# Performance work log

Measured on AMD Instinct MI355X. Metric: run time of the kernel, lower is better.

Reference implementation:

```python
import jax, jax.numpy as jnp
import numpy as np

D_MODEL = 512
NUM_HEADS = 8
DEPTH = D_MODEL // NUM_HEADS
PROJ_DIM = 256
SEQ_LEN = 4096
BATCH = 8


def _glorot(key, shape):
    fan_in, fan_out = shape[-2], shape[-1]
    limit = np.sqrt(6.0 / (fan_in + fan_out))
    return jax.random.uniform(key, shape, jnp.float32, -limit, limit)


def setup_inputs() -> dict:
    key = jax.random.key(0)
    ks = jax.random.split(key, 8)
    x = jax.random.normal(ks[0], (BATCH, SEQ_LEN, D_MODEL), jnp.float32)
    wq = _glorot(ks[1], (D_MODEL, D_MODEL))
    wk = _glorot(ks[2], (D_MODEL, D_MODEL))
    wv = _glorot(ks[3], (D_MODEL, D_MODEL))
    E = _glorot(ks[4], (NUM_HEADS, SEQ_LEN, PROJ_DIM))
    F = _glorot(ks[5], (NUM_HEADS, SEQ_LEN, PROJ_DIM))
    w_out = _glorot(ks[6], (D_MODEL, D_MODEL))
    b_out = jnp.zeros((D_MODEL,), jnp.float32)
    return {"x": x, "wq": wq, "wk": wk, "wv": wv, "E": E, "F": F,
            "w_out": w_out, "b_out": b_out}


def reference(x, wq, wk, wv, E, F, w_out, b_out):
    b, n, _ = x.shape
    # QKV projections + split heads -> [b, h, n, d]
    def split_heads(t):
        return t.reshape(b, n, NUM_HEADS, DEPTH).transpose(0, 2, 1, 3)
    q = split_heads(x @ wq)
    k = split_heads(x @ wk)
    v = split_heads(x @ wv)
    # Linformer low-rank projection of K/V along sequence: [b,h,r,d]
    k_proj = jnp.einsum('bhnd,hnr->bhrd', k, E)
    v_proj = jnp.einsum('bhnd,hnr->bhrd', v, F)
    scale = 1.0 / jnp.sqrt(jnp.asarray(DEPTH, jnp.float32))
    scores = jnp.einsum('bhnd,bhrd->bhnr', q, k_proj) * scale  # [b,h,n,r]
    attn = jax.nn.softmax(scores, axis=-1)
    out = jnp.einsum('bhnr,bhrd->bhnd', attn, v_proj)
    out = out.transpose(0, 2, 1, 3).reshape(b, n, D_MODEL)
    return out @ w_out + b_out
```

## Files before the change

kernel.cpp:

```cpp
#include <hip/hip_runtime.h>

typedef unsigned short u16;
typedef unsigned int   u32;
typedef __bf16 bf16x8 __attribute__((ext_vector_type(8)));
typedef float  f32x4  __attribute__((ext_vector_type(4)));
typedef u16    u16x4  __attribute__((ext_vector_type(4)));

#define DEV __device__ __forceinline__

DEV u16 f2bf(float f) {
    u32 u = __builtin_bit_cast(u32, f);
    u = (u + 0x7fffu + ((u >> 16) & 1u)) >> 16;
    return (u16)u;
}

DEV void gload16(const void* g, void* l) {
    __builtin_amdgcn_global_load_lds((const __attribute__((address_space(1))) u32*)g,
                                     (__attribute__((address_space(3))) u32*)l, 16, 0, 0);
}


__global__ __launch_bounds__(256) void k_cvt4(const float* __restrict__ in,
                                              u16* __restrict__ out, int n) {
    int i = ((int)blockIdx.x * 256 + (int)threadIdx.x) * 4;
    if (i < n) {
        float4 v = *(const float4*)(in + i);
        u16x4 o;
        o[0] = f2bf(v.x); o[1] = f2bf(v.y); o[2] = f2bf(v.z); o[3] = f2bf(v.w);
        *(u16x4*)(out + i) = o;
    }
}

__global__ __launch_bounds__(256) void k_wt(const float* __restrict__ wq, const float* __restrict__ wk,
                                            const float* __restrict__ wv, const float* __restrict__ wo,
                                            u16* __restrict__ wcatT, u16* __restrict__ woT) {
    int idx = (int)blockIdx.x * 256 + (int)threadIdx.x;
    if (idx < 786432) {
        int j = idx >> 9, k = idx & 511;
        const float* w = (j < 512) ? wq : ((j < 1024) ? wk : wv);
        wcatT[idx] = f2bf(w[k * 512 + (j & 511)]);
    } else {
        int t = idx - 786432;
        int j = t >> 9, k = t & 511;
        woT[t] = f2bf(wo[k * 512 + j]);
    }
}

__global__ __launch_bounds__(256) void k_tef(const float* __restrict__ E, const float* __restrict__ F,
                                             u16* __restrict__ Et, u16* __restrict__ Ft) {
    __shared__ u16 tile[64][65];
    const int t = threadIdx.x;
    const int bid = blockIdx.x;
    const int rt = bid & 3, ntl = (bid >> 2) & 63, h = (bid >> 8) & 7, which = bid >> 11;
    const float* src = (which ? F : E) + (size_t)h * 4096 * 256;
    u16* dst = (which ? Ft : Et) + (size_t)h * 256 * 4096;
    const int n0 = ntl * 64, r0 = rt * 64;
#pragma unroll
    for (int it = 0; it < 16; ++it) {
        const int idx = t + it * 256;
        const int nl = idx >> 6, rl = idx & 63;
        tile[nl][rl] = f2bf(src[(size_t)(n0 + nl) * 256 + r0 + rl]);
    }
    __syncthreads();
#pragma unroll
    for (int it = 0; it < 16; ++it) {
        const int idx = t + it * 256;
        const int rl = idx >> 6, nl = idx & 63;
        dst[(size_t)(r0 + rl) * 4096 + n0 + nl] = tile[nl][rl];
    }
}

template <int MODE>
__global__ __launch_bounds__(256) void k_gemm(const u16* __restrict__ A, const u16* __restrict__ Bm,
                                              u16* __restrict__ Qo, u16* __restrict__ Kt, u16* __restrict__ Vt,
                                              float* __restrict__ Of, const float* __restrict__ bias,
                                              int M, int N, int K) {
    __shared__ __attribute__((aligned(16))) char smem[32768];
    const int tid = threadIdx.x;
    const int lane = tid & 63, wid = tid >> 6;
    const int wr = wid >> 1, wc = wid & 1;
    const int g = lane >> 4, l16 = lane & 15;
    const int nM = M >> 7;
    const int bm = (int)blockIdx.x % nM, bn = (int)blockIdx.x / nM;
    const int m0 = bm << 7, n0 = bn << 7;

    f32x4 acc[4][4] = {};

    for (int k0 = 0; k0 < K; k0 += 64) {
#pragma unroll
        for (int c = 0; c < 4; ++c) {
            const int off = c * 4096 + tid * 16;
            const int row = off >> 7;
            const int sc = ((off >> 4) & 7) ^ (row & 7);
            gload16(A  + (size_t)(m0 + row) * K + (k0 + sc * 8), smem + off);
            gload16(Bm + (size_t)(n0 + row) * K + (k0 + sc * 8), smem + 16384 + off);
        }
        __syncthreads();
#pragma unroll
        for (int kk = 0; kk < 64; kk += 32) {
            bf16x8 av[4], bv[4];
#pragma unroll
            for (int m = 0; m < 4; ++m) {
                const int r = wr * 64 + m * 16 + l16;
                av[m] = *(const bf16x8*)(smem + r * 128 + ((kk * 2 + g * 16) ^ ((r & 7) << 4)));
            }
#pragma unroll
            for (int n = 0; n < 4; ++n) {
                const int r = wc * 64 + n * 16 + l16;
                bv[n] = *(const bf16x8*)(smem + 16384 + r * 128 + ((kk * 2 + g * 16) ^ ((r & 7) << 4)));
            }
#pragma unroll
            for (int m = 0; m < 4; ++m)
#pragma unroll
                for (int n = 0; n < 4; ++n)
                    acc[m][n] = __builtin_amdgcn_mfma_f32_16x16x32_bf16(av[m], bv[n], acc[m][n], 0, 0, 0);
        }
        __syncthreads();
    }

    if (MODE == 0) {
        if (n0 < 512) {
#pragma unroll
            for (int m = 0; m < 4; ++m)
#pragma unroll
                for (int n = 0; n < 4; ++n) {
                    const int col = n0 + wc * 64 + n * 16 + l16;
#pragma unroll
                    for (int i = 0; i < 4; ++i) {
                        const int row = m0 + wr * 64 + m * 16 + g * 4 + i;
                        Qo[(size_t)row * 512 + col] = f2bf(acc[m][n][i]);
                    }
                }
        } else {
            u16* dst = (n0 < 1024) ? Kt : Vt;
#pragma unroll
            for (int m = 0; m < 4; ++m)
#pragma unroll
                for (int n = 0; n < 4; ++n) {
                    const int col = (n0 + wc * 64 + n * 16 + l16) & 511;
                    const int h = col >> 6, d = col & 63;
                    const int rowb = m0 + wr * 64 + m * 16 + g * 4;
                    const int b = rowb >> 12, nn = rowb & 4095;
                    u16x4 pk;
#pragma unroll
                    for (int i = 0; i < 4; ++i) pk[i] = f2bf(acc[m][n][i]);
                    *(u16x4*)(dst + ((size_t)((b * 8 + h) * 64 + d)) * 4096 + nn) = pk;
                }
        }
    } else {
#pragma unroll
        for (int m = 0; m < 4; ++m)
#pragma unroll
            for (int n = 0; n < 4; ++n) {
                const int col = n0 + wc * 64 + n * 16 + l16;
                const float bb = bias[col];
#pragma unroll
                for (int i = 0; i < 4; ++i) {
                    const int row = m0 + wr * 64 + m * 16 + g * 4 + i;
                    Of[(size_t)row * N + col] = acc[m][n][i] + bb;
                }
            }
    }
}

__global__ __launch_bounds__(256) void k_proj(const u16* __restrict__ Et, const u16* __restrict__ Ft,
                                              const u16* __restrict__ Kt, const u16* __restrict__ Vt,
                                              u16* __restrict__ kp, u16* __restrict__ vpT) {
    __shared__ __attribute__((aligned(16))) char smem[24576];
    const int tid = threadIdx.x;
    const int lane = tid & 63, wid = tid >> 6;
    const int wr = wid >> 1, wc = wid & 1;
    const int g = lane >> 4, l16 = lane & 15;
    const int bid = blockIdx.x;
    const int mt = bid & 1, which = (bid >> 1) & 1, bh = bid >> 2;
    const int h = bh & 7;
    const u16* Ap = (which ? Ft : Et) + (size_t)h * 256 * 4096 + (size_t)mt * 128 * 4096;
    const u16* Bp = (which ? Vt : Kt) + (size_t)bh * 64 * 4096;

    f32x4 acc[4][2] = {};

    for (int k0 = 0; k0 < 4096; k0 += 64) {
#pragma unroll
        for (int c = 0; c < 4; ++c) {
            const int off = c * 4096 + tid * 16;
            const int row = off >> 7;
            const int sc = ((off >> 4) & 7) ^ (row & 7);
            gload16(Ap + (size_t)row * 4096 + (k0 + sc * 8), smem + off);
            if (c < 2)
                gload16(Bp + (size_t)row * 4096 + (k0 + sc * 8), smem + 16384 + off);
        }
        __syncthreads();
#pragma unroll
        for (int kk = 0; kk < 64; kk += 32) {
            bf16x8 av[4], bv[2];
#pragma unroll
            for (int m = 0; m < 4; ++m) {
                const int r = wr * 64 + m * 16 + l16;
                av[m] = *(const bf16x8*)(smem + r * 128 + ((kk * 2 + g * 16) ^ ((r & 7) << 4)));
            }
#pragma unroll
            for (int n = 0; n < 2; ++n) {
                const int r = wc * 32 + n * 16 + l16;
                bv[n] = *(const bf16x8*)(smem + 16384 + r * 128 + ((kk * 2 + g * 16) ^ ((r & 7) << 4)));
            }
#pragma unroll
            for (int m = 0; m < 4; ++m)
#pragma unroll
                for (int n = 0; n < 2; ++n)
                    acc[m][n] = __builtin_amdgcn_mfma_f32_16x16x32_bf16(av[m], bv[n], acc[m][n], 0, 0, 0);
        }
        __syncthreads();
    }

    if (which == 0) {
#pragma unroll
        for (int m = 0; m < 4; ++m)
#pragma unroll
            for (int n = 0; n < 2; ++n) {
                const int d = wc * 32 + n * 16 + l16;
#pragma unroll
                for (int i = 0; i < 4; ++i) {
                    const int rg = mt * 128 + wr * 64 + m * 16 + g * 4 + i;
                    kp[(size_t)bh * 16384 + rg * 64 + d] = f2bf(acc[m][n][i]);
                }
            }
    } else {
#pragma unroll
        for (int m = 0; m < 4; ++m)
#pragma unroll
            for (int n = 0; n < 2; ++n) {
                const int d = wc * 32 + n * 16 + l16;
                const int r4 = mt * 128 + wr * 64 + m * 16 + g * 4;
                u16x4 pk;
#pragma unroll
                for (int i = 0; i < 4; ++i) pk[i] = f2bf(acc[m][n][i]);
                *(u16x4*)(vpT + (size_t)bh * 16384 + d * 256 + r4) = pk;
            }
    }
}

__global__ __launch_bounds__(256) void k_flash(const u16* __restrict__ Q, const u16* __restrict__ kp,
                                               const u16* __restrict__ vpT, u16* __restrict__ ctx) {
    __shared__ __attribute__((aligned(16))) char smem[65536];
    const int tid = threadIdx.x;
    const int lane = tid & 63, w = tid >> 6;
    const int g = lane >> 4, l16 = lane & 15;
    const int bid = blockIdx.x;
    const int nt = bid & 63, bh = bid >> 6;
    const int b = bh >> 3, h = bh & 7;
    const int n0 = nt * 64;

#pragma unroll
    for (int c = 0; c < 8; ++c) {
        const int off = c * 4096 + tid * 16;
        {
            const int row = off >> 7;
            const int sc = ((off >> 4) & 7) ^ (row & 7);
            gload16(kp + (size_t)bh * 16384 + row * 64 + sc * 8, smem + off);
        }
        {
            const int row = off >> 9;
            const int sc = ((off >> 4) & 31) ^ (row & 7);
            gload16(vpT + (size_t)bh * 16384 + row * 256 + sc * 8, smem + 32768 + off);
        }
    }
    const size_t qbase = (size_t)(b * 4096 + n0 + w * 16 + l16) * 512 + h * 64 + g * 8;
    bf16x8 qf0 = *(const bf16x8*)(Q + qbase);
    bf16x8 qf1 = *(const bf16x8*)(Q + qbase + 32);
    __syncthreads();

    f32x4 s[16];
#pragma unroll
    for (int rt = 0; rt < 16; ++rt) {
        const int r = rt * 16 + l16;
        const int sw = (r & 7) << 4;
        bf16x8 kv0 = *(const bf16x8*)(smem + r * 128 + ((g * 16) ^ sw));
        bf16x8 kv1 = *(const bf16x8*)(smem + r * 128 + ((64 + g * 16) ^ sw));
        f32x4 z = {0.f, 0.f, 0.f, 0.f};
        z = __builtin_amdgcn_mfma_f32_16x16x32_bf16(qf0, kv0, z, 0, 0, 0);
        z = __builtin_amdgcn_mfma_f32_16x16x32_bf16(qf1, kv1, z, 0, 0, 0);
        s[rt] = z;
    }

    float mx[4] = {-1e30f, -1e30f, -1e30f, -1e30f};
#pragma unroll
    for (int rt = 0; rt < 16; ++rt)
#pragma unroll
        for (int i = 0; i < 4; ++i) {
            s[rt][i] *= 0.125f;
            mx[i] = fmaxf(mx[i], s[rt][i]);
        }
#pragma unroll
    for (int i = 0; i < 4; ++i) {
        mx[i] = fmaxf(mx[i], __shfl_xor(mx[i], 1));
        mx[i] = fmaxf(mx[i], __shfl_xor(mx[i], 2));
        mx[i] = fmaxf(mx[i], __shfl_xor(mx[i], 4));
        mx[i] = fmaxf(mx[i], __shfl_xor(mx[i], 8));
    }
    float sm[4] = {0.f, 0.f, 0.f, 0.f};
#pragma unroll
    for (int rt = 0; rt < 16; ++rt)
#pragma unroll
        for (int i = 0; i < 4; ++i) {
            float e = __expf(s[rt][i] - mx[i]);
            s[rt][i] = e;
            sm[i] += e;
        }
#pragma unroll
    for (int i = 0; i < 4; ++i) {
        sm[i] += __shfl_xor(sm[i], 1);
        sm[i] += __shfl_xor(sm[i], 2);
        sm[i] += __shfl_xor(sm[i], 4);
        sm[i] += __shfl_xor(sm[i], 8);
    }

    __syncthreads();

#pragma unroll
    for (int rt = 0; rt < 16; ++rt)
#pragma unroll
        for (int i = 0; i < 4; ++i) {
            const int nrow = g * 4 + i;
            const int byte = w * 8192 + nrow * 512 + ((rt * 32 + l16 * 2) ^ ((nrow & 7) << 4));
            *(u16*)(smem + byte) = f2bf(s[rt][i]);
        }
    bf16x8 af[8];
#pragma unroll
    for (int ks = 0; ks < 8; ++ks) {
        const int byte = w * 8192 + l16 * 512 + ((ks * 64 + g * 16) ^ ((l16 & 7) << 4));
        af[ks] = *(const bf16x8*)(smem + byte);
    }
    f32x4 o[4] = {};
#pragma unroll
    for (int dt = 0; dt < 4; ++dt)
#pragma unroll
        for (int ks = 0; ks < 8; ++ks) {
            const int row = dt * 16 + l16;
            const int byte = 32768 + row * 512 + ((ks * 64 + g * 16) ^ ((row & 7) << 4));
            bf16x8 bv = *(const bf16x8*)(smem + byte);
            o[dt] = __builtin_amdgcn_mfma_f32_16x16x32_bf16(af[ks], bv, o[dt], 0, 0, 0);
        }
    float rinv[4];
#pragma unroll
    for (int i = 0; i < 4; ++i) rinv[i] = 1.0f / sm[i];
#pragma unroll
    for (int dt = 0; dt < 4; ++dt)
#pragma unroll
        for (int i = 0; i < 4; ++i) {
            const int row = b * 4096 + n0 + w * 16 + g * 4 + i;
            const int col = h * 64 + dt * 16 + l16;
            ctx[(size_t)row * 512 + col] = f2bf(o[dt][i] * rinv[i]);
        }
}


extern "C" void kernel_launch(void* const* d_in, const int* in_sizes, int n_in,
                              void* d_out, int out_size, void* d_ws, size_t ws_size,
                              hipStream_t stream) {
    const float* x  = (const float*)d_in[0];
    const float* wq = (const float*)d_in[1];
    const float* wk = (const float*)d_in[2];
    const float* wv = (const float*)d_in[3];
    const float* E  = (const float*)d_in[4];
    const float* F  = (const float*)d_in[5];
    const float* wo = (const float*)d_in[6];
    const float* bo = (const float*)d_in[7];
    float* out = (float*)d_out;
    u16* ws = (u16*)d_ws;

    u16* xb    = ws;
    u16* Qm    = ws + 16777216;
    u16* Kt    = ws + 33554432;
    u16* Vt    = ws + 50331648;
    u16* Et    = ws + 67108864;
    u16* Ft    = ws + 75497472;
    u16* wcatT = ws + 83886080;
    u16* woT   = ws + 84672512;
    u16* kpB   = ws + 84934656;
    u16* vpT   = ws + 85983232;
    u16* ctx   = xb;

    k_cvt4<<<16384, 256, 0, stream>>>(x, xb, 16777216);
    k_wt<<<4096, 256, 0, stream>>>(wq, wk, wv, wo, wcatT, woT);
    k_tef<<<4096, 256, 0, stream>>>(E, F, Et, Ft);
    k_gemm<0><<<3072, 256, 0, stream>>>(xb, wcatT, Qm, Kt, Vt, nullptr, nullptr, 32768, 1536, 512);
    k_proj<<<256, 256, 0, stream>>>(Et, Ft, Kt, Vt, kpB, vpT);
    k_flash<<<4096, 256, 0, stream>>>(Qm, kpB, vpT, ctx);
    k_gemm<1><<<1024, 256, 0, stream>>>(ctx, woT, nullptr, nullptr, nullptr, out, bo, 32768, 512, 512);
}
```

Baseline: 400.6 us.

## Split-K Linformer projection, fuse prep kernels, remap GEMM tiles, add setprio

Splits the sequence-length reduction in k_proj into four chunks written as fp32 partials, then reduced and converted to bf16 by a new kernel, so the projection uses four times as many blocks. The three input-conversion kernels merge into one launch, and the weight transpose now uses an LDS tile for coalesced access. GEMM block indices are remapped so each XCD covers contiguous M tiles, and MFMA loops are wrapped in s_setprio. This adds an extra fp32 buffer pass and a reduction launch.

Measured after the change: 385.3 us. 3.8% less time.

```diff
diff --git a/kernel.cpp b/kernel.cpp
--- a/kernel.cpp
+++ b/kernel.cpp
@@ -19,54 +19,59 @@
                                      (__attribute__((address_space(3))) u32*)l, 16, 0, 0);
 }
 
-
-__global__ __launch_bounds__(256) void k_cvt4(const float* __restrict__ in,
-                                              u16* __restrict__ out, int n) {
-    int i = ((int)blockIdx.x * 256 + (int)threadIdx.x) * 4;
-    if (i < n) {
-        float4 v = *(const float4*)(in + i);
-        u16x4 o;
-        o[0] = f2bf(v.x); o[1] = f2bf(v.y); o[2] = f2bf(v.z); o[3] = f2bf(v.w);
-        *(u16x4*)(out + i) = o;
-    }
-}
-
-__global__ __launch_bounds__(256) void k_wt(const float* __restrict__ wq, const float* __restrict__ wk,
-                                            const float* __restrict__ wv, const float* __restrict__ wo,
-                                            u16* __restrict__ wcatT, u16* __restrict__ woT) {
-    int idx = (int)blockIdx.x * 256 + (int)threadIdx.x;
-    if (idx < 786432) {
-        int j = idx >> 9, k = idx & 511;
-        const float* w = (j < 512) ? wq : ((j < 1024) ? wk : wv);
-        wcatT[idx] = f2bf(w[k * 512 + (j & 511)]);
-    } else {
-        int t = idx - 786432;
-        int j = t >> 9, k = t & 511;
-        woT[t] = f2bf(wo[k * 512 + j]);
-    }
-}
-
-__global__ __launch_bounds__(256) void k_tef(const float* __restrict__ E, const float* __restrict__ F,
-                                             u16* __restrict__ Et, u16* __restrict__ Ft) {
+__global__ __launch_bounds__(256) void k_prep(const float* __restrict__ x,
+                                              const float* __restrict__ wq, const float* __restrict__ wk,
+                                              const float* __restrict__ wv, const float* __restrict__ wo,
+                                              const float* __restrict__ E, const float* __restrict__ F,
+                                              u16* __restrict__ xb, u16* __restrict__ wcatT, u16* __restrict__ woT,
+                                              u16* __restrict__ Et, u16* __restrict__ Ft) {
     __shared__ u16 tile[64][65];
     const int t = threadIdx.x;
     const int bid = blockIdx.x;
-    const int rt = bid & 3, ntl = (bid >> 2) & 63, h = (bid >> 8) & 7, which = bid >> 11;
-    const float* src = (which ? F : E) + (size_t)h * 4096 * 256;
-    u16* dst = (which ? Ft : Et) + (size_t)h * 256 * 4096;
-    const int n0 = ntl * 64, r0 = rt * 64;
-#pragma unroll
-    for (int it = 0; it < 16; ++it) {
-        const int idx = t + it * 256;
-        const int nl = idx >> 6, rl = idx & 63;
-        tile[nl][rl] = f2bf(src[(size_t)(n0 + nl) * 256 + r0 + rl]);
-    }
-    __syncthreads();
-#pragma unroll
-    for (int it = 0; it < 16; ++it) {
-        const int idx = t + it * 256;
-        const int rl = idx >> 6, nl = idx & 63;
-        dst[(size_t)(r0 + rl) * 4096 + n0 + nl] = tile[nl][rl];
+    if (bid < 16384) {
+        int i = (bid * 256 + t) * 4;
+        float4 v = *(const float4*)(x + i);
+        u16x4 o;
+        o[0] = f2bf(v.x); o[1] = f2bf(v.y); o[2] = f2bf(v.z); o[3] = f2bf(v.w);
+        *(u16x4*)(xb + i) = o;
+    } else if (bid < 20480) {
+        const int b2 = bid - 16384;
+        const int rt = b2 & 3, ntl = (b2 >> 2) & 63, h = (b2 >> 8) & 7, which = b2 >> 11;
+        const float* src = (which ? F : E) + (size_t)h * 4096 * 256;
+        u16* dst = (which ? Ft : Et) + (size_t)h * 256 * 4096;
+        const int n0 = ntl * 64, r0 = rt * 64;
+#pragma unroll
+        for (int it = 0; it < 16; ++it) {
+            const int idx = t + it * 256;
+            const int nl = idx >> 6, rl = idx & 63;
+            tile[nl][rl] = f2bf(src[(size_t)(n0 + nl) * 256 + r0 + rl]);
+        }
+        __syncthreads();
+#pragma unroll
+        for (int it = 0; it < 16; ++it) {
+            const int idx = t + it * 256;
+            const int rl = idx >> 6, nl = idx & 63;
+            dst[(size_t)(r0 + rl) * 4096 + n0 + nl] = tile[nl][rl];
+        }
+    } else {
+        const int b2 = bid - 20480;
+        const int mi = b2 >> 6, tix = b2 & 63;
+        const int jt = tix & 7, kt = tix >> 3;
+        const float* w = (mi == 0) ? wq : (mi == 1) ? wk : (mi == 2) ? wv : wo;
+        u16* dst = (mi < 3) ? (wcatT + mi * 262144) : woT;
+#pragma unroll
+        for (int it = 0; it < 16; ++it) {
+            const int idx = t + it * 256;
+            const int kl = idx >> 6, jl = idx & 63;
+            tile[kl][jl] = f2bf(w[(kt * 64 + kl) * 512 + jt * 64 + jl]);
+        }
+        __syncthreads();
+#pragma unroll
+        for (int it = 0; it < 16; ++it) {
+            const int idx = t + it * 256;
+            const int jl = idx >> 6, kl = idx & 63;
+            dst[(size_t)(jt * 64 + jl) * 512 + kt * 64 + kl] = tile[kl][jl];
+        }
     }
 }
 
@@ -80,8 +85,9 @@
     const int lane = tid & 63, wid = tid >> 6;
     const int wr = wid >> 1, wc = wid & 1;
     const int g = lane >> 4, l16 = lane & 15;
-    const int nM = M >> 7;
-    const int bm = (int)blockIdx.x % nM, bn = (int)blockIdx.x / nM;
+    const int bid = (int)blockIdx.x;
+    const int xcd = bid & 7, loc = bid >> 3;
+    const int bm = xcd * 32 + (loc & 31), bn = loc >> 5;
     const int m0 = bm << 7, n0 = bn << 7;
 
     f32x4 acc[4][4] = {};
@@ -109,11 +115,13 @@
                 const int r = wc * 64 + n * 16 + l16;
                 bv[n] = *(const bf16x8*)(smem + 16384 + r * 128 + ((kk * 2 + g * 16) ^ ((r & 7) << 4)));
             }
+            __builtin_amdgcn_s_setprio(1);
 #pragma unroll
             for (int m = 0; m < 4; ++m)
 #pragma unroll
                 for (int n = 0; n < 4; ++n)
                     acc[m][n] = __builtin_amdgcn_mfma_f32_16x16x32_bf16(av[m], bv[n], acc[m][n], 0, 0, 0);
+            __builtin_amdgcn_s_setprio(0);
         }
         __syncthreads();
     }
@@ -165,21 +173,23 @@
 
 __global__ __launch_bounds__(256) void k_proj(const u16* __restrict__ Et, const u16* __restrict__ Ft,
                                               const u16* __restrict__ Kt, const u16* __restrict__ Vt,
-                                              u16* __restrict__ kp, u16* __restrict__ vpT) {
+                                              float* __restrict__ pbuf) {
     __shared__ __attribute__((aligned(16))) char smem[24576];
     const int tid = threadIdx.x;
     const int lane = tid & 63, wid = tid >> 6;
     const int wr = wid >> 1, wc = wid & 1;
     const int g = lane >> 4, l16 = lane & 15;
     const int bid = blockIdx.x;
-    const int mt = bid & 1, which = (bid >> 1) & 1, bh = bid >> 2;
+    const int sp = bid >> 8, rest = bid & 255;
+    const int mt = rest & 1, which = (rest >> 1) & 1, bh = rest >> 2;
     const int h = bh & 7;
     const u16* Ap = (which ? Ft : Et) + (size_t)h * 256 * 4096 + (size_t)mt * 128 * 4096;
     const u16* Bp = (which ? Vt : Kt) + (size_t)bh * 64 * 4096;
 
     f32x4 acc[4][2] = {};
 
-    for (int k0 = 0; k0 < 4096; k0 += 64) {
+    const int kbeg = sp * 1024;
+    for (int k0 = kbeg; k0 < kbeg + 1024; k0 += 64) {
 #pragma unroll
         for (int c = 0; c < 4; ++c) {
             const int off = c * 4096 + tid * 16;
@@ -203,15 +213,18 @@
                 const int r = wc * 32 + n * 16 + l16;
                 bv[n] = *(const bf16x8*)(smem + 16384 + r * 128 + ((kk * 2 + g * 16) ^ ((r & 7) << 4)));
             }
+            __builtin_amdgcn_s_setprio(1);
 #pragma unroll
             for (int m = 0; m < 4; ++m)
 #pragma unroll
                 for (int n = 0; n < 2; ++n)
                     acc[m][n] = __builtin_amdgcn_mfma_f32_16x16x32_bf16(av[m], bv[n], acc[m][n], 0, 0, 0);
-        }
-        __syncthreads();
-    }
-
+            __builtin_amdgcn_s_setprio(0);
+        }
+        __syncthreads();
+    }
+
+    float* pb = pbuf + ((size_t)(sp * 2 + which) * 64 + bh) * 16384;
     if (which == 0) {
 #pragma unroll
         for (int m = 0; m < 4; ++m)
@@ -221,7 +234,7 @@
 #pragma unroll
                 for (int i = 0; i < 4; ++i) {
                     const int rg = mt * 128 + wr * 64 + m * 16 + g * 4 + i;
-                    kp[(size_t)bh * 16384 + rg * 64 + d] = f2bf(acc[m][n][i]);
+                    pb[rg * 64 + d] = acc[m][n][i];
                 }
             }
     } else {
@@ -231,12 +244,21 @@
             for (int n = 0; n < 2; ++n) {
                 const int d = wc * 32 + n * 16 + l16;
                 const int r4 = mt * 128 + wr * 64 + m * 16 + g * 4;
-                u16x4 pk;
-#pragma unroll
-                for (int i = 0; i < 4; ++i) pk[i] = f2bf(acc[m][n][i]);
-                *(u16x4*)(vpT + (size_t)bh * 16384 + d * 256 + r4) = pk;
-            }
-    }
+                *(f32x4*)(pb + d * 256 + r4) = acc[m][n];
+            }
+    }
+}
+
+__global__ __launch_bounds__(256) void k_preduce(const float* __restrict__ pbuf, u16* __restrict__ outkv) {
+    const int o = ((int)blockIdx.x * 256 + (int)threadIdx.x) * 4;
+    f32x4 s = *(const f32x4*)(pbuf + o);
+    s += *(const f32x4*)(pbuf + 2097152 + o);
+    s += *(const f32x4*)(pbuf + 4194304 + o);
+    s += *(const f32x4*)(pbuf + 6291456 + o);
+    u16x4 r;
+#pragma unroll
+    for (int i = 0; i < 4; ++i) r[i] = f2bf(s[i]);
+    *(u16x4*)(outkv + o) = r;
 }
 
 __global__ __launch_bounds__(256) void k_flash(const u16* __restrict__ Q, const u16* __restrict__ kp,
@@ -270,6 +292,7 @@
     __syncthreads();
 
     f32x4 s[16];
+    __builtin_amdgcn_s_setprio(1);
 #pragma unroll
     for (int rt = 0; rt < 16; ++rt) {
         const int r = rt * 16 + l16;
@@ -281,6 +304,7 @@
         z = __builtin_amdgcn_mfma_f32_16x16x32_bf16(qf1, kv1, z, 0, 0, 0);
         s[rt] = z;
     }
+    __builtin_amdgcn_s_setprio(0);
 
     float mx[4] = {-1e30f, -1e30f, -1e30f, -1e30f};
 #pragma unroll
@@ -331,6 +355,7 @@
         af[ks] = *(const bf16x8*)(smem + byte);
     }
     f32x4 o[4] = {};
+    __builtin_amdgcn_s_setprio(1);
 #pragma unroll
     for (int dt = 0; dt < 4; ++dt)
 #pragma unroll
@@ -340,6 +365,7 @@
             bf16x8 bv = *(const bf16x8*)(smem + byte);
             o[dt] = __builtin_amdgcn_mfma_f32_16x16x32_bf16(af[ks], bv, o[dt], 0, 0, 0);
         }
+    __builtin_amdgcn_s_setprio(0);
     float rinv[4];
 #pragma unroll
     for (int i = 0; i < 4; ++i) rinv[i] = 1.0f / sm[i];
@@ -378,13 +404,13 @@
     u16* woT   = ws + 84672512;
     u16* kpB   = ws + 84934656;
     u16* vpT   = ws + 85983232;
+    float* pbuf = (float*)xb;
     u16* ctx   = xb;
 
-    k_cvt4<<<16384, 256, 0, stream>>>(x, xb, 16777216);
-    k_wt<<<4096, 256, 0, stream>>>(wq, wk, wv, wo, wcatT, woT);
-    k_tef<<<4096, 256, 0, stream>>>(E, F, Et, Ft);
+    k_prep<<<20736, 256, 0, stream>>>(x, wq, wk, wv, wo, E, F, xb, wcatT, woT, Et, Ft);
     k_gemm<0><<<3072, 256, 0, stream>>>(xb, wcatT, Qm, Kt, Vt, nullptr, nullptr, 32768, 1536, 512);
-    k_proj<<<256, 256, 0, stream>>>(Et, Ft, Kt, Vt, kpB, vpT);
+    k_proj<<<1024, 256, 0, stream>>>(Et, Ft, Kt, Vt, pbuf);
+    k_preduce<<<2048, 256, 0, stream>>>(pbuf, kpB);
     k_flash<<<4096, 256, 0, stream>>>(Qm, kpB, vpT, ctx);
     k_gemm<1><<<1024, 256, 0, stream>>>(ctx, woT, nullptr, nullptr, nullptr, out, bo, 32768, 512, 512);
 }
```
